# Kernel optimization log

Measured on AMD Instinct MI355X. Metric: run time of the kernel, lower is better.

## Reference

```python
import jax, jax.numpy as jnp
import numpy as np

# static config (levels=4, CDA=False branch -> self_attn_4, scale=4, f=False)
SHAPES = [(80, 80), (40, 40), (20, 20), (10, 10)]
D = 256; NH = 8; NL = 4; NP = 4; DFF = 1024; DH = D // NH
L = sum(h * w for h, w in SHAPES)  # 8500
B = 1


def layer_norm(x, g, b, eps=1e-5):
    m = jnp.mean(x, axis=-1, keepdims=True)
    v = jnp.mean((x - m) ** 2, axis=-1, keepdims=True)
    return (x - m) * jax.lax.rsqrt(v + eps) * g + b


def ms_deform_attn_core(value, loc, attn):
    # value: [B, L, NH, DH]; loc: [B, Lq, NH, NL, NP, 2] in [0,1]; attn: [B, Lq, NH, NL, NP]
    Bq, Lq = loc.shape[0], loc.shape[1]
    out = jnp.zeros((Bq, NH, Lq, DH), value.dtype)
    start = 0
    for lvl, (Hl, Wl) in enumerate(SHAPES):
        v = value[:, start:start + Hl * Wl]          # [B, HW, NH, DH]
        start += Hl * Wl
        v = v.transpose(0, 2, 1, 3)                  # [B, NH, HW, DH]
        ll = loc[:, :, :, lvl]                       # [B, Lq, NH, NP, 2]
        # grid_sample semantics: align_corners=False, padding_mode='zeros'
        x = ll[..., 0] * Wl - 0.5
        y = ll[..., 1] * Hl - 0.5
        x0 = jnp.floor(x); y0 = jnp.floor(y)
        acc = jnp.zeros((Bq, NH, Lq, NP, DH), value.dtype)
        for dy in (0, 1):
            for dx in (0, 1):
                xi = x0 + dx; yi = y0 + dy
                w = (1.0 - jnp.abs(x - xi)) * (1.0 - jnp.abs(y - yi))  # [B,Lq,NH,NP]
                valid = (xi >= 0) & (xi < Wl) & (yi >= 0) & (yi < Hl)
                xi_c = jnp.clip(xi, 0, Wl - 1).astype(jnp.int32)
                yi_c = jnp.clip(yi, 0, Hl - 1).astype(jnp.int32)
                lin = (yi_c * Wl + xi_c).transpose(0, 2, 1, 3).reshape(Bq, NH, Lq * NP)
                g = jnp.take_along_axis(v, lin[..., None], axis=2).reshape(Bq, NH, Lq, NP, DH)
                wv = (w * valid.astype(w.dtype)).transpose(0, 2, 1, 3)[..., None]
                acc = acc + g * wv
        aw = attn[:, :, :, lvl].transpose(0, 2, 1, 3)[..., None]  # [B,NH,Lq,NP,1]
        out = out + jnp.sum(acc * aw, axis=3)
    return out.transpose(0, 2, 1, 3).reshape(Bq, Lq, NH * DH)


def setup_inputs():
    key = jax.random.key(0)
    ks = jax.random.split(key, 24)
    s = 0.02
    d = {}
    d['src'] = jax.random.normal(ks[0], (B, L, D), jnp.float32)
    d['pos'] = jax.random.normal(ks[1], (B, L, D), jnp.float32)
    d['reference_points'] = jax.random.uniform(ks[2], (B, L, NL, 2), jnp.float32)
    d['spatial_shapes'] = jnp.array(SHAPES, jnp.int32)
    d['level_start_index'] = jnp.array(np.cumsum([0] + [h * w for h, w in SHAPES[:-1]]), jnp.int32)
    d['scale'] = 4
    # MSDeformAttn params
    d['Wo'] = jax.random.normal(ks[3], (D, NH * NL * NP * 2), jnp.float32) * s
    d['bo'] = jax.random.normal(ks[4], (NH * NL * NP * 2,), jnp.float32) * s
    d['Wa'] = jax.random.normal(ks[5], (D, NH * NL * NP), jnp.float32) * s
    d['ba'] = jax.random.normal(ks[6], (NH * NL * NP,), jnp.float32) * s
    d['Wv'] = jax.random.normal(ks[7], (D, D), jnp.float32) * s
    d['bv'] = jnp.zeros((D,), jnp.float32)
    d['Wout'] = jax.random.normal(ks[8], (D, D), jnp.float32) * s
    d['bout'] = jnp.zeros((D,), jnp.float32)
    # FFN + LayerNorms
    d['W1'] = jax.random.normal(ks[9], (D, DFF), jnp.float32) * s
    d['b1'] = jnp.zeros((DFF,), jnp.float32)
    d['W2'] = jax.random.normal(ks[10], (DFF, D), jnp.float32) * s
    d['b2'] = jnp.zeros((D,), jnp.float32)
    d['g1'] = jnp.ones((D,), jnp.float32); d['be1'] = jnp.zeros((D,), jnp.float32)
    d['g2'] = jnp.ones((D,), jnp.float32); d['be2'] = jnp.zeros((D,), jnp.float32)
    return d


def reference(src, pos, reference_points, spatial_shapes, level_start_index, scale,
              Wo, bo, Wa, ba, Wv, bv, Wout, bout, W1, b1, W2, b2, g1, be1, g2, be2):
    Bq, Lq, _ = src.shape
    q = src + pos  # with_pos_embed
    # sampling offsets & attention weights (softmax over levels*points)
    off = (q @ Wo + bo).reshape(Bq, Lq, NH, NL, NP, 2)
    attn = jax.nn.softmax((q @ Wa + ba).reshape(Bq, Lq, NH, NL * NP), axis=-1)
    attn = attn.reshape(Bq, Lq, NH, NL, NP)
    value = (src @ Wv + bv).reshape(Bq, L, NH, DH)
    # offset normalizer is (W, H) per level
    normalizer = jnp.stack([spatial_shapes[:, 1], spatial_shapes[:, 0]], -1).astype(src.dtype)
    loc = reference_points[:, :, None, :, None, :] + off / normalizer[None, None, None, :, None, :]
    src2 = ms_deform_attn_core(value, loc, attn) @ Wout + bout
    # residual + norm1 (dropout = eval identity)
    x = layer_norm(src + src2, g1, be1)
    # FFN
    ffn = jax.nn.relu(x @ W1 + b1) @ W2 + b2
    x = layer_norm(x + ffn, g2, be2)
    return x
```

## Files before the change

### kernel.cpp

```cpp
#include <hip/hip_runtime.h>
#include <hip/hip_bf16.h>

#define D 256
#define NH 8
#define DH 32
#define NL 4
#define NP 4
#define DFF 1024
#define LTOT 8500

typedef __bf16 bf16x8 __attribute__((ext_vector_type(8)));
typedef float floatx4 __attribute__((ext_vector_type(4)));

__global__ void prep(const float* __restrict__ src, const float* __restrict__ pos,
                     __hip_bfloat16* __restrict__ qb, __hip_bfloat16* __restrict__ srcb, int n) {
    int i = blockIdx.x * blockDim.x + threadIdx.x;
    if (i < n) {
        float s = src[i];
        srcb[i] = __float2bfloat16(s);
        qb[i] = __float2bfloat16(s + pos[i]);
    }
}

__global__ void transpose_all(const float* W0, const float* W1_, const float* W2_,
                              const float* W3, const float* W4, const float* W5,
                              __hip_bfloat16* T0, __hip_bfloat16* T1, __hip_bfloat16* T2,
                              __hip_bfloat16* T3, __hip_bfloat16* T4, __hip_bfloat16* T5) {
    const float* W; __hip_bfloat16* T; int K, N;
    switch (blockIdx.z) {
        case 0: W = W0; T = T0; K = 256;  N = 256;  break;
        case 1: W = W1_; T = T1; K = 256; N = 128;  break;
        case 2: W = W2_; T = T2; K = 256; N = 256;  break;
        case 3: W = W3; T = T3; K = 256;  N = 256;  break;
        case 4: W = W4; T = T4; K = 256;  N = 1024; break;
        default: W = W5; T = T5; K = 1024; N = 256; break;
    }
    int bx = blockIdx.x, by = blockIdx.y;
    if (bx >= (N >> 5) || by >= (K >> 5)) return;
    __shared__ float t[32][33];
    int n0 = bx * 32, k0 = by * 32;
    int tx = threadIdx.x & 31, ty = threadIdx.x >> 5;
#pragma unroll
    for (int i = 0; i < 32; i += 8)
        t[ty + i][tx] = W[(size_t)(k0 + ty + i) * N + n0 + tx];
    __syncthreads();
#pragma unroll
    for (int i = 0; i < 32; i += 8)
        T[(size_t)(n0 + ty + i) * K + k0 + tx] = __float2bfloat16(t[tx][ty + i]);
}

template<int BM, int BN>
__global__ __launch_bounds__(256) void gemm_mfma(
    const __hip_bfloat16* __restrict__ A, const __hip_bfloat16* __restrict__ BT,
    const float* __restrict__ bias, float* __restrict__ Cf, __hip_bfloat16* __restrict__ Cb,
    int M, int N, int K, int relu) {
    constexpr int BK = 32;
    constexpr int LDA = BK + 8;
    __shared__ __hip_bfloat16 sA[BM * LDA];
    __shared__ __hip_bfloat16 sB[BN * LDA];

    int tid = threadIdx.x;
    int wave = tid >> 6, lane = tid & 63;
    int m0 = blockIdx.y * BM;
    int n0 = blockIdx.x * BN;
    constexpr int WM = BM / 2, WN = BN / 2;
    int wm = (wave >> 1) * WM;
    int wn = (wave & 1) * WN;
    constexpr int TM = WM / 16, TN = WN / 16;

    floatx4 acc[TM][TN];
#pragma unroll
    for (int i = 0; i < TM; i++)
#pragma unroll
        for (int j = 0; j < TN; j++)
#pragma unroll
            for (int e = 0; e < 4; e++) acc[i][j][e] = 0.f;

    constexpr int RA = BM / 64, RB = BN / 64;
    int rowT = tid >> 2;
    int c16 = tid & 3;
    int lrow = lane & 15;
    int lk = (lane >> 4) * 8;

    for (int k0 = 0; k0 < K; k0 += BK) {
#pragma unroll
        for (int r = 0; r < RA; r++) {
            int row = r * 64 + rowT;
            int grow = m0 + row; if (grow >= M) grow = M - 1;
            bf16x8 v = *(const bf16x8*)(A + (size_t)grow * K + k0 + c16 * 8);
            *(bf16x8*)(&sA[row * LDA + c16 * 8]) = v;
        }
#pragma unroll
        for (int r = 0; r < RB; r++) {
            int row = r * 64 + rowT;
            bf16x8 v = *(const bf16x8*)(BT + (size_t)(n0 + row) * K + k0 + c16 * 8);
            *(bf16x8*)(&sB[row * LDA + c16 * 8]) = v;
        }
        __syncthreads();

        bf16x8 af[TM], bfr[TN];
#pragma unroll
        for (int tm = 0; tm < TM; tm++)
            af[tm] = *(const bf16x8*)(&sA[(wm + tm * 16 + lrow) * LDA + lk]);
#pragma unroll
        for (int tn = 0; tn < TN; tn++)
            bfr[tn] = *(const bf16x8*)(&sB[(wn + tn * 16 + lrow) * LDA + lk]);
#pragma unroll
        for (int tm = 0; tm < TM; tm++)
#pragma unroll
            for (int tn = 0; tn < TN; tn++)
                acc[tm][tn] = __builtin_amdgcn_mfma_f32_16x16x32_bf16(af[tm], bfr[tn], acc[tm][tn], 0, 0, 0);
        __syncthreads();
    }

    int lcol = lane & 15;
    int lr4 = (lane >> 4) * 4;
#pragma unroll
    for (int tm = 0; tm < TM; tm++) {
#pragma unroll
        for (int i = 0; i < 4; i++) {
            int row = m0 + wm + tm * 16 + lr4 + i;
            if (row < M) {
#pragma unroll
                for (int tn = 0; tn < TN; tn++) {
                    int col = n0 + wn + tn * 16 + lcol;
                    float v = acc[tm][tn][i] + bias[col];
                    if (relu) v = fmaxf(v, 0.f);
                    if (Cf) Cf[(size_t)row * N + col] = v;
                    if (Cb) Cb[(size_t)row * N + col] = __float2bfloat16(v);
                }
            }
        }
    }
}

__global__ __launch_bounds__(256) void proj_fused(
    const __hip_bfloat16* __restrict__ qb, const __hip_bfloat16* __restrict__ srcb,
    const __hip_bfloat16* __restrict__ WoT, const __hip_bfloat16* __restrict__ WaT,
    const __hip_bfloat16* __restrict__ WvT,
    const float* __restrict__ bo, const float* __restrict__ ba, const float* __restrict__ bv,
    float* __restrict__ locb, float* __restrict__ attnb, __hip_bfloat16* __restrict__ valb,
    int M) {
    constexpr int BM = 64, BN = 64, BK = 32, K = 256;
    constexpr int LDA = BK + 8;
    __shared__ __hip_bfloat16 sA[BM * LDA];
    __shared__ __hip_bfloat16 sB[BN * LDA];

    int n0 = blockIdx.x * BN;
    int m0 = blockIdx.y * BM;

    const __hip_bfloat16* A;
    const __hip_bfloat16* BT;
    const float* bias;
    int ncol0, Nout;
    float* Cf; __hip_bfloat16* Cb;
    if (n0 < 256)      { A = qb;   BT = WoT; bias = bo; ncol0 = n0;       Nout = 256; Cf = locb;  Cb = nullptr; }
    else if (n0 < 384) { A = qb;   BT = WaT; bias = ba; ncol0 = n0 - 256; Nout = 128; Cf = attnb; Cb = nullptr; }
    else               { A = srcb; BT = WvT; bias = bv; ncol0 = n0 - 384; Nout = 256; Cf = nullptr; Cb = valb; }

    int tid = threadIdx.x;
    int wave = tid >> 6, lane = tid & 63;
    int wm = (wave >> 1) * 32;
    int wn = (wave & 1) * 32;

    floatx4 acc[2][2];
#pragma unroll
    for (int i = 0; i < 2; i++)
#pragma unroll
        for (int j = 0; j < 2; j++)
#pragma unroll
            for (int e = 0; e < 4; e++) acc[i][j][e] = 0.f;

    int rowT = tid >> 2, c16 = tid & 3;
    int lrow = lane & 15, lk = (lane >> 4) * 8;

    for (int k0 = 0; k0 < K; k0 += BK) {
        {
            int grow = m0 + rowT; if (grow >= M) grow = M - 1;
            *(bf16x8*)(&sA[rowT * LDA + c16 * 8]) =
                *(const bf16x8*)(A + (size_t)grow * K + k0 + c16 * 8);
            *(bf16x8*)(&sB[rowT * LDA + c16 * 8]) =
                *(const bf16x8*)(BT + (size_t)(ncol0 + rowT) * K + k0 + c16 * 8);
        }
        __syncthreads();
        bf16x8 af[2], bfr[2];
#pragma unroll
        for (int t = 0; t < 2; t++) {
            af[t]  = *(const bf16x8*)(&sA[(wm + t * 16 + lrow) * LDA + lk]);
            bfr[t] = *(const bf16x8*)(&sB[(wn + t * 16 + lrow) * LDA + lk]);
        }
#pragma unroll
        for (int tm = 0; tm < 2; tm++)
#pragma unroll
            for (int tn = 0; tn < 2; tn++)
                acc[tm][tn] = __builtin_amdgcn_mfma_f32_16x16x32_bf16(af[tm], bfr[tn], acc[tm][tn], 0, 0, 0);
        __syncthreads();
    }

    int lcol = lane & 15, lr4 = (lane >> 4) * 4;
#pragma unroll
    for (int tm = 0; tm < 2; tm++) {
#pragma unroll
        for (int i = 0; i < 4; i++) {
            int row = m0 + wm + tm * 16 + lr4 + i;
            if (row < M) {
#pragma unroll
                for (int tn = 0; tn < 2; tn++) {
                    int col = ncol0 + wn + tn * 16 + lcol;
                    float v = acc[tm][tn][i] + bias[col];
                    if (Cf) Cf[(size_t)row * Nout + col] = v;
                    else    Cb[(size_t)row * Nout + col] = __float2bfloat16(v);
                }
            }
        }
    }
}

__global__ void softmax_loc(const float* __restrict__ refp, float* __restrict__ attn,
                            float* __restrict__ loc) {
    int g = blockIdx.x * blockDim.x + threadIdx.x;
    if (g >= LTOT * NH) return;
    int q = g >> 3, h = g & 7;

    float* lg = attn + q * (NH * NL * NP) + h * (NL * NP);
    float v[16];
    float mx = -1e30f;
#pragma unroll
    for (int j = 0; j < 16; j++) { v[j] = lg[j]; mx = fmaxf(mx, v[j]); }
    float s = 0.f;
#pragma unroll
    for (int j = 0; j < 16; j++) { v[j] = __expf(v[j] - mx); s += v[j]; }
    float inv = 1.f / s;
#pragma unroll
    for (int j = 0; j < 16; j++) lg[j] = v[j] * inv;

    float* lc = loc + q * 256 + h * 32;
#pragma unroll
    for (int l = 0; l < 4; l++) {
        float nv = (float)(80 >> l);
        float rx = refp[(q * 4 + l) * 2 + 0];
        float ry = refp[(q * 4 + l) * 2 + 1];
#pragma unroll
        for (int p = 0; p < 4; p++) {
            int o = (l * 4 + p) * 2;
            lc[o + 0] = rx + lc[o + 0] / nv;
            lc[o + 1] = ry + lc[o + 1] / nv;
        }
    }
}

__global__ __launch_bounds__(256) void deform(const __hip_bfloat16* __restrict__ value,
                                              const float* __restrict__ loc,
                                              const float* __restrict__ attn,
                                              __hip_bfloat16* __restrict__ out) {
    __shared__ float wS[2][8][16][4];
    __shared__ int   aS[2][8][16][4];
    int tid = threadIdx.x;
    int q0 = blockIdx.x * 2;

    {
        int sub = tid >> 7, h = (tid >> 4) & 7, pp = tid & 15;
        int q = q0 + sub;
        int l = pp >> 2;
        const int starts[4] = {0, 6400, 8000, 8400};
        int Wl = 80 >> l;
        float lx = loc[q * 256 + h * 32 + pp * 2 + 0];
        float ly = loc[q * 256 + h * 32 + pp * 2 + 1];
        float a  = attn[q * 128 + h * 16 + pp];
        float x = lx * (float)Wl - 0.5f;
        float y = ly * (float)Wl - 0.5f;
        float x0f = floorf(x), y0f = floorf(y);
        float fx = x - x0f, fy = y - y0f;
        int x0 = (int)x0f, y0 = (int)y0f;
        float wts[4] = {(1.f - fx) * (1.f - fy), fx * (1.f - fy),
                        (1.f - fx) * fy,         fx * fy};
        int st = starts[l];
#pragma unroll
        for (int t = 0; t < 4; t++) {
            int xi = x0 + (t & 1), yi = y0 + (t >> 1);
            bool valid = (xi >= 0) & (xi < Wl) & (yi >= 0) & (yi < Wl);
            int xc = min(max(xi, 0), Wl - 1), yc = min(max(yi, 0), Wl - 1);
            wS[sub][h][pp][t] = valid ? wts[t] * a : 0.f;
            aS[sub][h][pp][t] = (st + yc * Wl + xc) * 512 + h * 64;
        }
    }
    __syncthreads();

    int sub = tid >> 7, h = (tid >> 4) & 7, l16 = tid & 15;
    int q = q0 + sub;
    const char* vb = (const char*)value;
    int lo = l16 * 4;
    float acc0 = 0.f, acc1 = 0.f;
#pragma unroll
    for (int p = 0; p < 16; p++) {
        floatx4 w = *(const floatx4*)&wS[sub][h][p][0];
        int4 av = *(const int4*)&aS[sub][h][p][0];
        unsigned u0 = *(const unsigned*)(vb + av.x + lo);
        unsigned u1 = *(const unsigned*)(vb + av.y + lo);
        unsigned u2 = *(const unsigned*)(vb + av.z + lo);
        unsigned u3 = *(const unsigned*)(vb + av.w + lo);
        acc0 += w[0] * __uint_as_float(u0 << 16);
        acc1 += w[0] * __uint_as_float(u0 & 0xffff0000u);
        acc0 += w[1] * __uint_as_float(u1 << 16);
        acc1 += w[1] * __uint_as_float(u1 & 0xffff0000u);
        acc0 += w[2] * __uint_as_float(u2 << 16);
        acc1 += w[2] * __uint_as_float(u2 & 0xffff0000u);
        acc0 += w[3] * __uint_as_float(u3 << 16);
        acc1 += w[3] * __uint_as_float(u3 & 0xffff0000u);
    }
    __hip_bfloat162 o;
    o.x = __float2bfloat16(acc0);
    o.y = __float2bfloat16(acc1);
    *(__hip_bfloat162*)(out + q * 256 + h * 32 + l16 * 2) = o;
}

__global__ __launch_bounds__(256) void gemm_ln(
    const __hip_bfloat16* __restrict__ A, const __hip_bfloat16* __restrict__ BT,
    const float* __restrict__ bias, const float* __restrict__ resid,
    const float* __restrict__ g, const float* __restrict__ be,
    float* __restrict__ outf, __hip_bfloat16* __restrict__ outb,
    int M, int K) {
    constexpr int BM = 32, BK = 32, LDA = BK + 8;
    __shared__ __hip_bfloat16 sA[BM * LDA];
    __shared__ __hip_bfloat16 sB[256 * LDA];
    __shared__ float psum[4][32], psq[4][32], mS[32], rS[32];

    int tid = threadIdx.x;
    int wave = tid >> 6, lane = tid & 63;
    int m0 = blockIdx.x * BM;

    floatx4 acc[2][4];
#pragma unroll
    for (int i = 0; i < 2; i++)
#pragma unroll
        for (int j = 0; j < 4; j++)
#pragma unroll
            for (int e = 0; e < 4; e++) acc[i][j][e] = 0.f;

    int rowT = tid >> 2, c16 = tid & 3;
    int lrow = lane & 15, lk = (lane >> 4) * 8;

    for (int k0 = 0; k0 < K; k0 += BK) {
        if (tid < 128) {
            int grow = m0 + rowT; if (grow >= M) grow = M - 1;
            *(bf16x8*)(&sA[rowT * LDA + c16 * 8]) =
                *(const bf16x8*)(A + (size_t)grow * K + k0 + c16 * 8);
        }
#pragma unroll
        for (int r = 0; r < 4; r++) {
            int row = r * 64 + rowT;
            *(bf16x8*)(&sB[row * LDA + c16 * 8]) =
                *(const bf16x8*)(BT + (size_t)row * K + k0 + c16 * 8);
        }
        __syncthreads();
        bf16x8 af[2], bfr[4];
#pragma unroll
        for (int tm = 0; tm < 2; tm++)
            af[tm] = *(const bf16x8*)(&sA[(tm * 16 + lrow) * LDA + lk]);
#pragma unroll
        for (int tn = 0; tn < 4; tn++)
            bfr[tn] = *(const bf16x8*)(&sB[(wave * 64 + tn * 16 + lrow) * LDA + lk]);
#pragma unroll
        for (int tm = 0; tm < 2; tm++)
#pragma unroll
            for (int tn = 0; tn < 4; tn++)
                acc[tm][tn] = __builtin_amdgcn_mfma_f32_16x16x32_bf16(af[tm], bfr[tn], acc[tm][tn], 0, 0, 0);
        __syncthreads();
    }

    int lcol = lane & 15, quad = lane >> 4;
    float v[2][4][4];
#pragma unroll
    for (int tm = 0; tm < 2; tm++) {
#pragma unroll
        for (int i = 0; i < 4; i++) {
            int row = tm * 16 + quad * 4 + i;
            int grow = m0 + row; if (grow >= M) grow = M - 1;
#pragma unroll
            for (int tn = 0; tn < 4; tn++) {
                int col = wave * 64 + tn * 16 + lcol;
                v[tm][tn][i] = acc[tm][tn][i] + bias[col] + resid[(size_t)grow * 256 + col];
            }
        }
    }

#pragma unroll
    for (int tm = 0; tm < 2; tm++) {
#pragma unroll
        for (int i = 0; i < 4; i++) {
            float s = 0.f, s2 = 0.f;
#pragma unroll
            for (int tn = 0; tn < 4; tn++) { float x = v[tm][tn][i]; s += x; s2 += x * x; }
#pragma unroll
            for (int m = 1; m < 16; m <<= 1) {
                s  += __shfl_xor(s, m, 64);
                s2 += __shfl_xor(s2, m, 64);
            }
            if (lcol == 0) {
                int row = tm * 16 + quad * 4 + i;
                psum[wave][row] = s;
                psq[wave][row]  = s2;
            }
        }
    }
    __syncthreads();
    if (tid < 32) {
        float s  = psum[0][tid] + psum[1][tid] + psum[2][tid] + psum[3][tid];
        float s2 = psq[0][tid]  + psq[1][tid]  + psq[2][tid]  + psq[3][tid];
        float m = s * (1.f / 256.f);
        float var = fmaxf(s2 * (1.f / 256.f) - m * m, 0.f);
        mS[tid] = m;
        rS[tid] = rsqrtf(var + 1e-5f);
    }
    __syncthreads();

#pragma unroll
    for (int tm = 0; tm < 2; tm++) {
#pragma unroll
        for (int i = 0; i < 4; i++) {
            int row = tm * 16 + quad * 4 + i;
            int grow = m0 + row;
            if (grow < M) {
                float m = mS[row], r = rS[row];
#pragma unroll
                for (int tn = 0; tn < 4; tn++) {
                    int col = wave * 64 + tn * 16 + lcol;
                    float o = (v[tm][tn][i] - m) * r * g[col] + be[col];
                    outf[(size_t)grow * 256 + col] = o;
                    if (outb) outb[(size_t)grow * 256 + col] = __float2bfloat16(o);
                }
            }
        }
    }
}

extern "C" void kernel_launch(void* const* d_in, const int* in_sizes, int n_in,
                              void* d_out, int out_size, void* d_ws, size_t ws_size,
                              hipStream_t stream) {
    const float* src  = (const float*)d_in[0];
    const float* pos  = (const float*)d_in[1];
    const float* refp = (const float*)d_in[2];
    const float* Wo   = (const float*)d_in[6];
    const float* bo   = (const float*)d_in[7];
    const float* Wa   = (const float*)d_in[8];
    const float* ba   = (const float*)d_in[9];
    const float* Wv   = (const float*)d_in[10];
    const float* bv   = (const float*)d_in[11];
    const float* Wout = (const float*)d_in[12];
    const float* bout = (const float*)d_in[13];
    const float* W1   = (const float*)d_in[14];
    const float* b1   = (const float*)d_in[15];
    const float* W2   = (const float*)d_in[16];
    const float* b2   = (const float*)d_in[17];
    const float* g1   = (const float*)d_in[18];
    const float* be1  = (const float*)d_in[19];
    const float* g2   = (const float*)d_in[20];
    const float* be2  = (const float*)d_in[21];
    float* out = (float*)d_out;
    char* ws = (char*)d_ws;

    __hip_bfloat16* WoT   = (__hip_bfloat16*)(ws + 0);
    __hip_bfloat16* WaT   = (__hip_bfloat16*)(ws + 131072);
    __hip_bfloat16* WvT   = (__hip_bfloat16*)(ws + 196608);
    __hip_bfloat16* WoutT = (__hip_bfloat16*)(ws + 327680);
    __hip_bfloat16* W1T   = (__hip_bfloat16*)(ws + 458752);
    __hip_bfloat16* W2T   = (__hip_bfloat16*)(ws + 983040);
    __hip_bfloat16* qb    = (__hip_bfloat16*)(ws + 1507328);
    __hip_bfloat16* srcb  = (__hip_bfloat16*)(ws + 5859328);
    float*          locb  = (float*)(ws + 10211328);
    float*          attnb = (float*)(ws + 18915328);
    __hip_bfloat16* valb  = (__hip_bfloat16*)(ws + 23267328);
    __hip_bfloat16* hb    = (__hip_bfloat16*)(ws + 31971328);
    __hip_bfloat16* aob  = qb;
    float*          x1   = locb;
    __hip_bfloat16* x1b  = srcb;

    int n = LTOT * D;
    prep<<<(n + 255) / 256, 256, 0, stream>>>(src, pos, qb, srcb, n);
    transpose_all<<<dim3(32, 32, 6), 256, 0, stream>>>(Wo, Wa, Wv, Wout, W1, W2,
                                                       WoT, WaT, WvT, WoutT, W1T, W2T);

    proj_fused<<<dim3(10, 133), 256, 0, stream>>>(qb, srcb, WoT, WaT, WvT, bo, ba, bv,
                                                  locb, attnb, valb, LTOT);

    softmax_loc<<<(LTOT * NH + 255) / 256, 256, 0, stream>>>(refp, attnb, locb);
    deform<<<4250, 256, 0, stream>>>(valb, locb, attnb, aob);

    gemm_ln<<<266, 256, 0, stream>>>(aob, WoutT, bout, src, g1, be1, x1, x1b, LTOT, 256);
    gemm_mfma<128, 128><<<dim3(8, 67), 256, 0, stream>>>(x1b, W1T, b1, nullptr, hb, LTOT, 1024, 256, 1);
    gemm_ln<<<266, 256, 0, stream>>>(hb, W2T, b2, x1, g2, be2, out, nullptr, LTOT, 1024);
}
```

Baseline: 224.8 us.

## Fuse softmax and location normalisation into deform kernel, vectorise prep and transpose

Removes the separate softmax_loc kernel and computes the per-head softmax (via wave shuffles) and the sampling-location normalisation inside the deform kernel. This avoids a launch and a read-modify-write of the attention and location buffers. Deform now handles 4 queries per block, with each thread loading 8 bytes (4 bf16 channels) per corner instead of 4. The prep kernel is vectorised to float4 loads with packed bf16 stores. transpose_all uses a flat 1D grid so it no longer launches empty blocks.

```diff
diff --git a/kernel.cpp b/kernel.cpp
--- a/kernel.cpp
+++ b/kernel.cpp
@@ -1,5 +1,6 @@
 #include <hip/hip_runtime.h>
 #include <hip/hip_bf16.h>
+#include <string.h>
 
 #define D 256
 #define NH 8
@@ -12,22 +13,37 @@
 typedef __bf16 bf16x8 __attribute__((ext_vector_type(8)));
 typedef float floatx4 __attribute__((ext_vector_type(4)));
 
+__device__ inline unsigned bpack(float a, float b) {
+    __hip_bfloat16 ha = __float2bfloat16(a), hb = __float2bfloat16(b);
+    unsigned short ua, ub;
+    memcpy(&ua, &ha, 2); memcpy(&ub, &hb, 2);
+    return (unsigned)ua | ((unsigned)ub << 16);
+}
+
 __global__ void prep(const float* __restrict__ src, const float* __restrict__ pos,
-                     __hip_bfloat16* __restrict__ qb, __hip_bfloat16* __restrict__ srcb, int n) {
+                     unsigned* __restrict__ qb, unsigned* __restrict__ srcb, int n4) {
     int i = blockIdx.x * blockDim.x + threadIdx.x;
-    if (i < n) {
-        float s = src[i];
-        srcb[i] = __float2bfloat16(s);
-        qb[i] = __float2bfloat16(s + pos[i]);
-    }
+    if (i >= n4) return;
+    float4 s = *(const float4*)(src + i * 4);
+    float4 p = *(const float4*)(pos + i * 4);
+    uint2 sb, qb2;
+    sb.x = bpack(s.x, s.y); sb.y = bpack(s.z, s.w);
+    qb2.x = bpack(s.x + p.x, s.y + p.y); qb2.y = bpack(s.z + p.z, s.w + p.w);
+    *(uint2*)(srcb + i * 2) = sb;
+    *(uint2*)(qb + i * 2) = qb2;
 }
 
 __global__ void transpose_all(const float* W0, const float* W1_, const float* W2_,
                               const float* W3, const float* W4, const float* W5,
                               __hip_bfloat16* T0, __hip_bfloat16* T1, __hip_bfloat16* T2,
                               __hip_bfloat16* T3, __hip_bfloat16* T4, __hip_bfloat16* T5) {
+    const int cum[7] = {0, 64, 96, 160, 224, 480, 736};
+    int id = blockIdx.x;
+    int mi = 0;
+    while (id >= cum[mi + 1]) mi++;
+    int lid = id - cum[mi];
     const float* W; __hip_bfloat16* T; int K, N;
-    switch (blockIdx.z) {
+    switch (mi) {
         case 0: W = W0; T = T0; K = 256;  N = 256;  break;
         case 1: W = W1_; T = T1; K = 256; N = 128;  break;
         case 2: W = W2_; T = T2; K = 256; N = 256;  break;
@@ -35,10 +51,9 @@
         case 4: W = W4; T = T4; K = 256;  N = 1024; break;
         default: W = W5; T = T5; K = 1024; N = 256; break;
     }
-    int bx = blockIdx.x, by = blockIdx.y;
-    if (bx >= (N >> 5) || by >= (K >> 5)) return;
+    int ntx = N >> 5;
+    int n0 = (lid % ntx) * 32, k0 = (lid / ntx) * 32;
     __shared__ float t[32][33];
-    int n0 = bx * 32, k0 = by * 32;
     int tx = threadIdx.x & 31, ty = threadIdx.x >> 5;
 #pragma unroll
     for (int i = 0; i < 32; i += 8)
@@ -216,102 +231,86 @@
     }
 }
 
-__global__ void softmax_loc(const float* __restrict__ refp, float* __restrict__ attn,
-                            float* __restrict__ loc) {
-    int g = blockIdx.x * blockDim.x + threadIdx.x;
-    if (g >= LTOT * NH) return;
-    int q = g >> 3, h = g & 7;
-
-    float* lg = attn + q * (NH * NL * NP) + h * (NL * NP);
-    float v[16];
-    float mx = -1e30f;
-#pragma unroll
-    for (int j = 0; j < 16; j++) { v[j] = lg[j]; mx = fmaxf(mx, v[j]); }
-    float s = 0.f;
-#pragma unroll
-    for (int j = 0; j < 16; j++) { v[j] = __expf(v[j] - mx); s += v[j]; }
-    float inv = 1.f / s;
-#pragma unroll
-    for (int j = 0; j < 16; j++) lg[j] = v[j] * inv;
-
-    float* lc = loc + q * 256 + h * 32;
-#pragma unroll
-    for (int l = 0; l < 4; l++) {
-        float nv = (float)(80 >> l);
-        float rx = refp[(q * 4 + l) * 2 + 0];
-        float ry = refp[(q * 4 + l) * 2 + 1];
-#pragma unroll
-        for (int p = 0; p < 4; p++) {
-            int o = (l * 4 + p) * 2;
-            lc[o + 0] = rx + lc[o + 0] / nv;
-            lc[o + 1] = ry + lc[o + 1] / nv;
-        }
-    }
-}
-
 __global__ __launch_bounds__(256) void deform(const __hip_bfloat16* __restrict__ value,
-                                              const float* __restrict__ loc,
-                                              const float* __restrict__ attn,
+                                              const float* __restrict__ locraw,
+                                              const float* __restrict__ logits,
+                                              const float* __restrict__ refp,
                                               __hip_bfloat16* __restrict__ out) {
-    __shared__ float wS[2][8][16][4];
-    __shared__ int   aS[2][8][16][4];
+    __shared__ float wS[4][8][16][4];
+    __shared__ int   aS[4][8][16][4];
     int tid = threadIdx.x;
-    int q0 = blockIdx.x * 2;
+    int q0 = blockIdx.x * 4;
 
     {
-        int sub = tid >> 7, h = (tid >> 4) & 7, pp = tid & 15;
+        int sub = tid >> 6, h = (tid >> 3) & 7, t8 = tid & 7;
         int q = q0 + sub;
-        int l = pp >> 2;
+        const float* lg = logits + q * 128 + h * 16;
+        float l0 = lg[t8], l1 = lg[t8 + 8];
+        float mx = fmaxf(l0, l1);
+#pragma unroll
+        for (int m = 1; m < 8; m <<= 1) mx = fmaxf(mx, __shfl_xor(mx, m, 64));
+        float e0 = __expf(l0 - mx), e1 = __expf(l1 - mx);
+        float s = e0 + e1;
+#pragma unroll
+        for (int m = 1; m < 8; m <<= 1) s += __shfl_xor(s, m, 64);
+        float inv = 1.f / s;
+
         const int starts[4] = {0, 6400, 8000, 8400};
-        int Wl = 80 >> l;
-        float lx = loc[q * 256 + h * 32 + pp * 2 + 0];
-        float ly = loc[q * 256 + h * 32 + pp * 2 + 1];
-        float a  = attn[q * 128 + h * 16 + pp];
-        float x = lx * (float)Wl - 0.5f;
-        float y = ly * (float)Wl - 0.5f;
-        float x0f = floorf(x), y0f = floorf(y);
-        float fx = x - x0f, fy = y - y0f;
-        int x0 = (int)x0f, y0 = (int)y0f;
-        float wts[4] = {(1.f - fx) * (1.f - fy), fx * (1.f - fy),
-                        (1.f - fx) * fy,         fx * fy};
-        int st = starts[l];
-#pragma unroll
-        for (int t = 0; t < 4; t++) {
-            int xi = x0 + (t & 1), yi = y0 + (t >> 1);
-            bool valid = (xi >= 0) & (xi < Wl) & (yi >= 0) & (yi < Wl);
-            int xc = min(max(xi, 0), Wl - 1), yc = min(max(yi, 0), Wl - 1);
-            wS[sub][h][pp][t] = valid ? wts[t] * a : 0.f;
-            aS[sub][h][pp][t] = (st + yc * Wl + xc) * 512 + h * 64;
+#pragma unroll
+        for (int j = 0; j < 2; j++) {
+            int pp = t8 + 8 * j;
+            float a = (j ? e1 : e0) * inv;
+            int l = pp >> 2;
+            int Wl = 80 >> l;
+            float nv = (float)Wl;
+            float rx = refp[q * 8 + l * 2 + 0];
+            float ry = refp[q * 8 + l * 2 + 1];
+            float lx = rx + locraw[q * 256 + h * 32 + pp * 2 + 0] / nv;
+            float ly = ry + locraw[q * 256 + h * 32 + pp * 2 + 1] / nv;
+            float x = lx * nv - 0.5f;
+            float y = ly * nv - 0.5f;
+            float x0f = floorf(x), y0f = floorf(y);
+            float fx = x - x0f, fy = y - y0f;
+            int x0 = (int)x0f, y0 = (int)y0f;
+            float wts[4] = {(1.f - fx) * (1.f - fy), fx * (1.f - fy),
+                            (1.f - fx) * fy,         fx * fy};
+            int st = starts[l];
+#pragma unroll
+            for (int t = 0; t < 4; t++) {
+                int xi = x0 + (t & 1), yi = y0 + (t >> 1);
+                bool valid = (xi >= 0) & (xi < Wl) & (yi >= 0) & (yi < Wl);
+                int xc = min(max(xi, 0), Wl - 1), yc = min(max(yi, 0), Wl - 1);
+                wS[sub][h][pp][t] = valid ? wts[t] * a : 0.f;
+                aS[sub][h][pp][t] = (st + yc * Wl + xc) * 512 + h * 64;
+            }
         }
     }
     __syncthreads();
 
-    int sub = tid >> 7, h = (tid >> 4) & 7, l16 = tid & 15;
+    int sub = tid >> 6, h = (tid >> 3) & 7, l8 = tid & 7;
     int q = q0 + sub;
     const char* vb = (const char*)value;
-    int lo = l16 * 4;
-    float acc0 = 0.f, acc1 = 0.f;
+    int lo = l8 * 8;
+    float a0 = 0.f, a1 = 0.f, a2 = 0.f, a3 = 0.f;
 #pragma unroll
     for (int p = 0; p < 16; p++) {
         floatx4 w = *(const floatx4*)&wS[sub][h][p][0];
         int4 av = *(const int4*)&aS[sub][h][p][0];
-        unsigned u0 = *(const unsigned*)(vb + av.x + lo);
-        unsigned u1 = *(const unsigned*)(vb + av.y + lo);
-        unsigned u2 = *(const unsigned*)(vb + av.z + lo);
-        unsigned u3 = *(const unsigned*)(vb + av.w + lo);
-        acc0 += w[0] * __uint_as_float(u0 << 16);
-        acc1 += w[0] * __uint_as_float(u0 & 0xffff0000u);
-        acc0 += w[1] * __uint_as_float(u1 << 16);
-        acc1 += w[1] * __uint_as_float(u1 & 0xffff0000u);
-        acc0 += w[2] * __uint_as_float(u2 << 16);
-        acc1 += w[2] * __uint_as_float(u2 & 0xffff0000u);
-        acc0 += w[3] * __uint_as_float(u3 << 16);
-        acc1 += w[3] * __uint_as_float(u3 & 0xffff0000u);
-    }
-    __hip_bfloat162 o;
-    o.x = __float2bfloat16(acc0);
-    o.y = __float2bfloat16(acc1);
-    *(__hip_bfloat162*)(out + q * 256 + h * 32 + l16 * 2) = o;
+#pragma unroll
+        for (int t = 0; t < 4; t++) {
+            int ad = (t == 0) ? av.x : (t == 1) ? av.y : (t == 2) ? av.z : av.w;
+            uint2 u = *(const uint2*)(vb + ad + lo);
+            float wt = w[t];
+            a0 += wt * __uint_as_float(u.x << 16);
+            a1 += wt * __uint_as_float(u.x & 0xffff0000u);
+            a2 += wt * __uint_as_float(u.y << 16);
+            a3 += wt * __uint_as_float(u.y & 0xffff0000u);
+        }
+    }
+    uint2 o;
+    o.x = bpack(a0, a1);
+    o.y = bpack(a2, a3);
+    *(uint2*)((char*)out + q * 512 + h * 64 + l8 * 8) = o;
 }
 
 __global__ __launch_bounds__(256) void gemm_ln(
@@ -475,16 +474,14 @@
     float*          x1   = locb;
     __hip_bfloat16* x1b  = srcb;
 
-    int n = LTOT * D;
-    prep<<<(n + 255) / 256, 256, 0, stream>>>(src, pos, qb, srcb, n);
-    transpose_all<<<dim3(32, 32, 6), 256, 0, stream>>>(Wo, Wa, Wv, Wout, W1, W2,
-                                                       WoT, WaT, WvT, WoutT, W1T, W2T);
+    prep<<<2125, 256, 0, stream>>>(src, pos, (unsigned*)qb, (unsigned*)srcb, LTOT * D / 4);
+    transpose_all<<<736, 256, 0, stream>>>(Wo, Wa, Wv, Wout, W1, W2,
+                                           WoT, WaT, WvT, WoutT, W1T, W2T);
 
     proj_fused<<<dim3(10, 133), 256, 0, stream>>>(qb, srcb, WoT, WaT, WvT, bo, ba, bv,
                                                   locb, attnb, valb, LTOT);
 
-    softmax_loc<<<(LTOT * NH + 255) / 256, 256, 0, stream>>>(refp, attnb, locb);
-    deform<<<4250, 256, 0, stream>>>(valb, locb, attnb, aob);
+    deform<<<2125, 256, 0, stream>>>(valb, locb, attnb, refp, aob);
 
     gemm_ln<<<266, 256, 0, stream>>>(aob, WoutT, bout, src, g1, be1, x1, x1b, LTOT, 256);
     gemm_mfma<128, 128><<<dim3(8, 67), 256, 0, stream>>>(x1b, W1T, b1, nullptr, hb, LTOT, 1024, 256, 1);
```

New measurement: 219.7 us. 2.2% less time.
